# Kernel optimization log

Hardware: AMD Instinct MI355X
Metric: run time of the kernel (lower is better)

Reference implementation:

```python
import jax, jax.numpy as jnp
import numpy as np

# dims
B, S, LC, K, CE, L, WE, H = 64, 512, 16, 3, 10, 32, 200, 200
V, A, T = 50000, 128, 64
LP = LC + K - 1  # padded word length (pad_word adds (K-1)/2 on each side)
D_IN = WE + L    # LSTM input dim = 232


def setup_inputs() -> dict:
    key = jax.random.key(0)
    ks = jax.random.split(key, 16)
    f = lambda k, shp: jax.random.normal(k, shp, dtype=jnp.float32) * 0.05
    return {
        "char_ids": jax.random.randint(ks[0], (B, S, LP), 0, A),
        "word_ids": jax.random.randint(ks[1], (B, S), 0, V),
        "word_emb": f(ks[2], (V, WE)),
        "char_emb": f(ks[3], (A, CE)),
        "conv_w": f(ks[4], (L, K * CE)),   # Conv1d(1, l, K*CE) == linear 30->32
        "conv_b": f(ks[5], (L,)),
        "w_ih_f": f(ks[6], (4 * H, D_IN)),
        "w_hh_f": f(ks[7], (4 * H, H)),
        "b_ih_f": f(ks[8], (4 * H,)),
        "b_hh_f": f(ks[9], (4 * H,)),
        "w_ih_b": f(ks[10], (4 * H, D_IN)),
        "w_hh_b": f(ks[11], (4 * H, H)),
        "b_ih_b": f(ks[12], (4 * H,)),
        "b_hh_b": f(ks[13], (4 * H,)),
        "out_w": f(ks[14], (T, 2 * H)),
        "out_b": f(ks[15], (T,)),
    }


def _lstm(x, w_ih, w_hh, b_ih, b_hh, reverse):
    # x: [S, B, D]; PyTorch gate order i, f, g, o
    def step(carry, x_t):
        h, c = carry
        g = x_t @ w_ih.T + b_ih + h @ w_hh.T + b_hh
        i, f, gg, o = jnp.split(g, 4, axis=-1)
        c = jax.nn.sigmoid(f) * c + jax.nn.sigmoid(i) * jnp.tanh(gg)
        h = jax.nn.sigmoid(o) * jnp.tanh(c)
        return (h, c), h

    b = x.shape[1]
    init = (jnp.zeros((b, H), x.dtype), jnp.zeros((b, H), x.dtype))
    _, hs = jax.lax.scan(step, init, x, reverse=reverse)
    return hs  # [S, B, H]


def reference(char_ids, word_ids, word_emb, char_emb, conv_w, conv_b,
              w_ih_f, w_hh_f, b_ih_f, b_hh_f,
              w_ih_b, w_hh_b, b_ih_b, b_hh_b,
              out_w, out_b):
    # per-word char CNN + max-pool, fully batched over (B, S, windows)
    ce = char_emb[char_ids]                                    # [B,S,LP,CE]
    # sliding K-char windows, flattened to K*CE (== original x_hat construction)
    win = jnp.concatenate([ce[:, :, k:k + LC] for k in range(K)], axis=-1)  # [B,S,LC,K*CE]
    phi = jnp.einsum('bswd,ld->bswl', win, conv_w) + conv_b    # tiny conv == linear
    char_repr = phi.max(axis=2)                                # max-pool over positions -> [B,S,L]

    combined = jnp.concatenate([word_emb[word_ids], char_repr], axis=-1)  # [B,S,232]
    x = combined.reshape(S, B, D_IN)  # faithful to original .view (reshape, not transpose)

    hf = _lstm(x, w_ih_f, w_hh_f, b_ih_f, b_hh_f, reverse=False)
    hb = _lstm(x, w_ih_b, w_hh_b, b_ih_b, b_hh_b, reverse=True)
    lstm_out = jnp.concatenate([hf, hb], axis=-1)              # [S,B,2H]  (dropout: eval mode)

    tag_space = lstm_out.reshape(B, S, 2 * H) @ out_w.T + out_b  # faithful .view back
    return jax.nn.log_softmax(tag_space, axis=1)  # original normalizes over dim=1 (seq axis)
```

## Files before the change

kernel.cpp:

```cpp
#include <hip/hip_runtime.h>
#include <hip/hip_bf16.h>
#include <math.h>

constexpr int B_ = 64, S_ = 512, LP_ = 18, CE_ = 10, LF_ = 32;
constexpr int WE_ = 200, H_ = 200, T_ = 64;
constexpr int N_ = B_ * S_;
constexpr int KP_ = 256;
constexpr int G4_ = 800;
constexpr int NG_ = 1600;
constexpr int NGP_ = 1664;
constexpr float L2E_ = 1.4426950408889634f;

typedef short short8 __attribute__((ext_vector_type(8)));
typedef float f32x4 __attribute__((ext_vector_type(4)));

__device__ __forceinline__ ushort bf16bits(float v) {
  return __bfloat16_as_ushort(__float2bfloat16(v));
}
__device__ __forceinline__ float bf2f(ushort u) {
  return __uint_as_float(((uint)u) << 16);
}
__device__ __forceinline__ float exp2fast(float x) {
  float r; asm("v_exp_f32 %0, %1" : "=v"(r) : "v"(x)); return r;
}
__device__ __forceinline__ float sig2(float y) {
  return __builtin_amdgcn_rcpf(1.f + exp2fast(-y));
}

__global__ __launch_bounds__(256) void k_build_x(
    const int* __restrict__ char_ids, const int* __restrict__ word_ids,
    const float* __restrict__ word_emb, const float* __restrict__ char_emb,
    const float* __restrict__ conv_w, const float* __restrict__ conv_b,
    ushort* __restrict__ Xb)
{
  __shared__ float ce[4][LP_ * CE_];
  const int wave = threadIdx.x >> 6, lane = threadIdx.x & 63;
  const int n = blockIdx.x * 4 + wave;

  for (int i = lane; i < LP_ * CE_; i += 64) {
    int c = char_ids[n * LP_ + i / CE_];
    ce[wave][i] = char_emb[c * CE_ + (i % CE_)];
  }
  const float* we = word_emb + (size_t)word_ids[n] * WE_;
  ushort* xr = Xb + (size_t)n * KP_;
  if (lane < 50) {
    float4 p = *(const float4*)(we + lane * 4);
    ushort4 o;
    o.x = bf16bits(p.x); o.y = bf16bits(p.y); o.z = bf16bits(p.z); o.w = bf16bits(p.w);
    *(ushort4*)(xr + lane * 4) = o;
  }
  if (lane < KP_ - WE_ - LF_) xr[WE_ + LF_ + lane] = 0;
  __syncthreads();

  const int f = lane & 31, half = lane >> 5;
  float cw[30];
  #pragma unroll
  for (int i = 0; i < 30; ++i) cw[i] = conv_w[f * 30 + i];
  float m = -1e30f;
  for (int w = half * 8; w < half * 8 + 8; ++w) {
    float acc = 0.f;
    #pragma unroll
    for (int i = 0; i < 30; ++i) acc += ce[wave][w * CE_ + i] * cw[i];
    m = fmaxf(m, acc);
  }
  m = fmaxf(m, __shfl_xor(m, 32));
  if (half == 0) xr[WE_ + f] = bf16bits(m + conv_b[f]);
}

__global__ __launch_bounds__(64) void k_pack_w(
    const float* __restrict__ w_ih_f, const float* __restrict__ w_ih_b,
    const float* __restrict__ b_ih_f, const float* __restrict__ b_hh_f,
    const float* __restrict__ b_ih_b, const float* __restrict__ b_hh_b,
    ushort* __restrict__ Wb, float* __restrict__ biasc)
{
  const int r = blockIdx.x;
  if (r >= NG_) {
    for (int c = threadIdx.x; c < KP_; c += 64) Wb[(size_t)r * KP_ + c] = 0;
    if (threadIdx.x == 0) biasc[r] = 0.f;
    return;
  }
  const int rl = r < G4_ ? r : r - G4_;
  const int gate = rl / 200;
  const float sc = (gate == 2) ? 2.f * L2E_ : L2E_;
  const float* src = r < G4_ ? w_ih_f + (size_t)rl * 232 : w_ih_b + (size_t)rl * 232;
  for (int c = threadIdx.x; c < KP_; c += 64)
    Wb[(size_t)r * KP_ + c] = (c < 232) ? bf16bits(src[c] * sc) : (ushort)0;
  if (threadIdx.x == 0)
    biasc[r] = sc * (r < G4_ ? (b_ih_f[rl] + b_hh_f[rl]) : (b_ih_b[rl] + b_hh_b[rl]));
}

__global__ __launch_bounds__(64) void k_pack_wo(
    const float* __restrict__ out_w, ushort* __restrict__ Wo)
{
  const int r = blockIdx.x;
  for (int k = threadIdx.x; k < 416; k += 64)
    Wo[(size_t)r * 416 + k] = (k < 400) ? bf16bits(out_w[(size_t)r * 400 + k]) : (ushort)0;
}

__global__ __launch_bounds__(512) void k_gemm_proj(
    const ushort* __restrict__ Xb, const ushort* __restrict__ Wb,
    const float* __restrict__ biasc, ushort* __restrict__ Gc)
{
  __shared__ __align__(16) char smem[131072];
  const int tid = threadIdx.x;
  const int lane = tid & 63, w = tid >> 6;
  const int wr = w >> 2, wc = w & 3;
  const int colbase = blockIdx.x * 128;
  const int rowbase = blockIdx.y * 128;

  const char* Ag = (const char*)(Xb + (size_t)rowbase * KP_);
  const char* Bg = (const char*)(Wb + (size_t)colbase * KP_);
  #pragma unroll
  for (int it = 0; it < 8; ++it) {
    int slot = it * 512 + tid;
    int row = slot >> 5, c16 = slot & 31;
    int src = row * 512 + c16 * 16;
    int dst = row * 512 + ((c16 * 16) ^ ((row & 7) << 4));
    *(short8*)(smem + dst) = *(const short8*)(Ag + src);
    *(short8*)(smem + 65536 + dst) = *(const short8*)(Bg + src);
  }
  __syncthreads();

  f32x4 acc[4][2] = {};
  #pragma unroll
  for (int kk = 0; kk < 8; ++kk) {
    const int kb = kk * 64 + (lane >> 4) * 16;
    short8 a[4], b[2];
    #pragma unroll
    for (int m = 0; m < 4; ++m) {
      int ar = wr * 64 + m * 16 + (lane & 15);
      a[m] = *(const short8*)(smem + ar * 512 + (kb ^ ((ar & 7) << 4)));
    }
    #pragma unroll
    for (int n = 0; n < 2; ++n) {
      int bc = wc * 32 + n * 16 + (lane & 15);
      b[n] = *(const short8*)(smem + 65536 + bc * 512 + (kb ^ ((bc & 7) << 4)));
    }
    #pragma unroll
    for (int m = 0; m < 4; ++m)
      #pragma unroll
      for (int n = 0; n < 2; ++n)
        acc[m][n] = __builtin_amdgcn_mfma_f32_16x16x32_bf16(a[m], b[n], acc[m][n], 0, 0, 0);
  }
  __syncthreads();

  float* Cs = (float*)smem;
  #pragma unroll
  for (int m = 0; m < 4; ++m)
    #pragma unroll
    for (int n = 0; n < 2; ++n)
      #pragma unroll
      for (int i = 0; i < 4; ++i) {
        int r = wr * 64 + m * 16 + (lane >> 4) * 4 + i;
        int c = wc * 32 + n * 16 + (lane & 15);
        Cs[r * 132 + c] = acc[m][n][i];
      }
  __syncthreads();

  const int r = tid >> 2, cg = (tid & 3) * 32;
  ushort ob[32];
  #pragma unroll
  for (int j = 0; j < 32; ++j)
    ob[j] = bf16bits(Cs[r * 132 + cg + j] + biasc[colbase + cg + j]);
  const int colg = colbase + cg;
  ushort* dst = Gc + (size_t)(rowbase + r) * NG_ + colg;
  #pragma unroll
  for (int v = 0; v < 4; ++v)
    if (colg + v * 8 < NG_)
      *(short8*)(dst + v * 8) = *(short8*)(ob + v * 8);
}

__global__ __launch_bounds__(1024) void k_lstm(
    const ushort* __restrict__ Gc,
    const float* __restrict__ w_hh_f, const float* __restrict__ w_hh_b,
    ushort* __restrict__ hf, ushort* __restrict__ hb)
{
  __shared__ ushort h_lds[2][16][232];
  __shared__ __align__(16) char wlds45[2][65536];
  __shared__ __align__(16) char wlds6[17408];

  const int tid = threadIdx.x;
  const int lane = tid & 63, w = tid >> 6;
  const int lo = lane & 15, hi = lane >> 4;
  const bool hiHalf = lo >= 8;
  const int dir = blockIdx.x >> 3, grp = blockIdx.x & 7;
  const float* Whh = dir ? w_hh_b : w_hh_f;
  ushort* hout = dir ? hb : hf;

  for (int i = tid; i < 2 * 16 * 232; i += 1024) ((ushort*)h_lds)[i] = 0;
  if (tid < 256) ((uint*)(wlds6 + 16384))[tid] = 0;

  const int s = w;
  const int off = s < 12 ? 12 * s : 144 + 16 * (s - 12);
  const int cnt = s < 12 ? 12 : 16;
  const int rl  = min(cnt, 200 - off);

  short8 wreg[4][4];
  #pragma unroll
  for (int g = 0; g < 4; ++g) {
    const float sc = (g == 2) ? 2.f * L2E_ : L2E_;
    const float* wr = Whh + (size_t)(g * 200 + off + lo) * 200;
    const bool rowok = lo < rl;
    const int gid = s * 4 + g;
    #pragma unroll
    for (int kt = 0; kt < 7; ++kt) {
      const int k0 = kt * 32 + hi * 8;
      float v[8];
      if (rowok && k0 < 200) {
        float4 p0 = *(const float4*)(wr + k0);
        float4 p1 = *(const float4*)(wr + k0 + 4);
        v[0] = p0.x; v[1] = p0.y; v[2] = p0.z; v[3] = p0.w;
        v[4] = p1.x; v[5] = p1.y; v[6] = p1.z; v[7] = p1.w;
      } else {
        #pragma unroll
        for (int j = 0; j < 8; ++j) v[j] = 0.f;
      }
      short8 fr;
      #pragma unroll
      for (int j = 0; j < 8; ++j) fr[j] = (short)bf16bits(v[j] * sc);
      if (kt < 4) wreg[g][kt] = fr;
      else if (kt < 6) *(short8*)(wlds45[kt - 4] + gid * 1024 + lane * 16) = fr;
      else if (hi == 0) *(short8*)(wlds6 + gid * 256 + lo * 16) = fr;
    }
  }

  float c2_[2] = {0.f, 0.f};

  const int rowsel = lo & 7;
  const int step0 = dir ? (S_ - 1) : 0;
  const ushort* gpp = Gc + (size_t)(step0 * 64 + grp * 8 + rowsel) * NG_ + dir * G4_ + off + hi * 4;
  ushort* sp = hout + (size_t)(step0 * 64 + grp * 8 + rowsel) * H_ + off + hi * 4 + (hiHalf ? 2 : 0);
  const ptrdiff_t gstep = (dir ? -64 : 64) * (ptrdiff_t)NG_;
  const ptrdiff_t hstep = (dir ? -64 : 64) * (ptrdiff_t)H_;
  const bool cellok = (hi * 4 < rl);
  const int hwoff = rowsel * 464 + off * 2 + hi * 8 + (hiHalf ? 4 : 0);

  const char* base45a = wlds45[0] + s * 4096 + lane * 16;
  const char* base45b = wlds45[1] + s * 4096 + lane * 16;
  const char* base6   = wlds6 + ((hi == 0) ? (s * 1024 + lo * 16) : (16384 + lo * 16));

  __syncthreads();

  #pragma unroll 2
  for (int t = 0; t < S_; ++t) {
    const ushort (*HR)[232] = h_lds[t & 1];
    ushort (*HW)[232] = h_lds[(t & 1) ^ 1];

    uint2 pre[4];
    #pragma unroll
    for (int g = 0; g < 4; ++g)
      pre[g] = *(const uint2*)(gpp + g * 200);

    __builtin_amdgcn_s_setprio(1);
    f32x4 acc[4] = {};
    const char* hrow = (const char*)HR + lo * 464 + hi * 16;
    #pragma unroll
    for (int kt = 0; kt < 7; ++kt) {
      short8 hfr = *(const short8*)(hrow + kt * 64);
      if (kt < 4) {
        #pragma unroll
        for (int g = 0; g < 4; ++g)
          acc[g] = __builtin_amdgcn_mfma_f32_16x16x32_bf16(wreg[g][kt], hfr, acc[g], 0, 0, 0);
      } else if (kt == 4) {
        #pragma unroll
        for (int g = 0; g < 4; ++g) {
          short8 wk = *(const short8*)(base45a + g * 1024);
          acc[g] = __builtin_amdgcn_mfma_f32_16x16x32_bf16(wk, hfr, acc[g], 0, 0, 0);
        }
      } else if (kt == 5) {
        #pragma unroll
        for (int g = 0; g < 4; ++g) {
          short8 wk = *(const short8*)(base45b + g * 1024);
          acc[g] = __builtin_amdgcn_mfma_f32_16x16x32_bf16(wk, hfr, acc[g], 0, 0, 0);
        }
      } else {
        #pragma unroll
        for (int g = 0; g < 4; ++g) {
          short8 wk = *(const short8*)(base6 + g * 256);
          acc[g] = __builtin_amdgcn_mfma_f32_16x16x32_bf16(wk, hfr, acc[g], 0, 0, 0);
        }
      }
    }
    __builtin_amdgcn_s_setprio(0);

    const uint ui = hiHalf ? pre[0].y : pre[0].x;
    const uint uf = hiHalf ? pre[1].y : pre[1].x;
    const uint ug = hiHalf ? pre[2].y : pre[2].x;
    const uint uo = hiHalf ? pre[3].y : pre[3].x;
    const float aI0 = hiHalf ? acc[0][2] : acc[0][0];
    const float aI1 = hiHalf ? acc[0][3] : acc[0][1];
    const float aF0 = hiHalf ? acc[1][2] : acc[1][0];
    const float aF1 = hiHalf ? acc[1][3] : acc[1][1];
    const float aG0 = hiHalf ? acc[2][2] : acc[2][0];
    const float aG1 = hiHalf ? acc[2][3] : acc[2][1];
    const float aO0 = hiHalf ? acc[3][2] : acc[3][0];
    const float aO1 = hiHalf ? acc[3][3] : acc[3][1];

    float hv0, hv1;
    {
      float gi = aI0 + bf2f((ushort)ui);
      float gf = aF0 + bf2f((ushort)uf);
      float gg = aG0 + bf2f((ushort)ug);
      float go = aO0 + bf2f((ushort)uo);
      float cn = sig2(gf) * c2_[0] + sig2(gi) * (2.f * sig2(gg) - 1.f);
      c2_[0] = cn;
      hv0 = sig2(go) * (2.f * sig2(cn * (2.f * L2E_)) - 1.f);
    }
    {
      float gi = aI1 + bf2f((ushort)(ui >> 16));
      float gf = aF1 + bf2f((ushort)(uf >> 16));
      float gg = aG1 + bf2f((ushort)(ug >> 16));
      float go = aO1 + bf2f((ushort)(uo >> 16));
      float cn = sig2(gf) * c2_[1] + sig2(gi) * (2.f * sig2(gg) - 1.f);
      c2_[1] = cn;
      hv1 = sig2(go) * (2.f * sig2(cn * (2.f * L2E_)) - 1.f);
    }
    const uint pkw = (uint)bf16bits(hv0) | ((uint)bf16bits(hv1) << 16);
    if (cellok) {
      *(uint*)((char*)HW + hwoff) = pkw;
    }

    __syncthreads();

    if (cellok) *(uint*)sp = pkw;
    sp += hstep;
    gpp += gstep;
  }
}

__global__ __launch_bounds__(256) void k_out(
    const ushort* __restrict__ hf, const ushort* __restrict__ hb,
    const ushort* __restrict__ Wo, const float* __restrict__ out_b,
    float* __restrict__ tag)
{
  __shared__ __align__(16) char smem[131072];
  const int tid = threadIdx.x;
  const int lane = tid & 63, w = tid >> 6;
  const int n0 = blockIdx.x * 64;

  for (int s2 = tid; s2 < 64 * 52; s2 += 256) {
    int row = s2 / 52, c = s2 % 52;
    short8 v = {};
    if (c < 25)      v = *(const short8*)(hf + (size_t)(n0 + row) * H_ + c * 8);
    else if (c < 50) v = *(const short8*)(hb + (size_t)(n0 + row) * H_ + (c - 25) * 8);
    *(short8*)(smem + row * 1024 + ((c ^ (row & 7)) << 4)) = v;
  }
  for (int s2 = tid; s2 < 64 * 52; s2 += 256) {
    int row = s2 / 52, c = s2 % 52;
    short8 v = *(const short8*)(Wo + (size_t)row * 416 + c * 8);
    *(short8*)(smem + 65536 + row * 1024 + ((c ^ (row & 7)) << 4)) = v;
  }
  __syncthreads();

  const int lo4 = lane & 15, hi4 = lane >> 4;
  f32x4 acc[4] = {};
  #pragma unroll
  for (int kt = 0; kt < 13; ++kt) {
    const int ck = kt * 4 + hi4;
    const int ar = w * 16 + lo4;
    short8 a = *(const short8*)(smem + ar * 1024 + ((ck ^ (ar & 7)) << 4));
    #pragma unroll
    for (int n = 0; n < 4; ++n) {
      const int br = n * 16 + lo4;
      short8 b = *(const short8*)(smem + 65536 + br * 1024 + ((ck ^ (br & 7)) << 4));
      acc[n] = __builtin_amdgcn_mfma_f32_16x16x32_bf16(a, b, acc[n], 0, 0, 0);
    }
  }
  #pragma unroll
  for (int n = 0; n < 4; ++n) {
    const int col = n * 16 + lo4;
    const float bb = out_b[col];
    #pragma unroll
    for (int i = 0; i < 4; ++i) {
      const int row = hi4 * 4 + i;
      tag[(size_t)(n0 + w * 16 + row) * T_ + col] = acc[n][i] + bb;
    }
  }
}

__global__ __launch_bounds__(256) void k_lsm(
    const float* __restrict__ tag, float* __restrict__ out)
{
  __shared__ float red[4][T_];
  __shared__ float lse[T_];
  const int b = blockIdx.x;
  const int tt = threadIdx.x & 63, ch = threadIdx.x >> 6;
  const float* tb = tag + (size_t)b * S_ * T_;

  float m = -1e30f;
  for (int s = ch * 128; s < ch * 128 + 128; ++s) m = fmaxf(m, tb[s * T_ + tt]);
  red[ch][tt] = m;
  __syncthreads();
  if (ch == 0)
    lse[tt] = fmaxf(fmaxf(red[0][tt], red[1][tt]), fmaxf(red[2][tt], red[3][tt]));
  __syncthreads();
  m = lse[tt];
  float sum = 0.f;
  for (int s = ch * 128; s < ch * 128 + 128; ++s) sum += __expf(tb[s * T_ + tt] - m);
  __syncthreads();
  red[ch][tt] = sum;
  __syncthreads();
  if (ch == 0)
    lse[tt] = m + logf(red[0][tt] + red[1][tt] + red[2][tt] + red[3][tt]);
  __syncthreads();
  const float l = lse[tt];
  float* ob = out + (size_t)b * S_ * T_;
  for (int s = ch * 128; s < ch * 128 + 128; ++s) ob[s * T_ + tt] = tb[s * T_ + tt] - l;
}

extern "C" void kernel_launch(void* const* d_in, const int* in_sizes, int n_in,
                              void* d_out, int out_size, void* d_ws, size_t ws_size,
                              hipStream_t stream) {
  const int*   char_ids = (const int*)d_in[0];
  const int*   word_ids = (const int*)d_in[1];
  const float* word_emb = (const float*)d_in[2];
  const float* char_emb = (const float*)d_in[3];
  const float* conv_w   = (const float*)d_in[4];
  const float* conv_b   = (const float*)d_in[5];
  const float* w_ih_f   = (const float*)d_in[6];
  const float* w_hh_f   = (const float*)d_in[7];
  const float* b_ih_f   = (const float*)d_in[8];
  const float* b_hh_f   = (const float*)d_in[9];
  const float* w_ih_b   = (const float*)d_in[10];
  const float* w_hh_b   = (const float*)d_in[11];
  const float* b_ih_b   = (const float*)d_in[12];
  const float* b_hh_b   = (const float*)d_in[13];
  const float* out_w    = (const float*)d_in[14];
  const float* out_b    = (const float*)d_in[15];

  char* ws = (char*)d_ws;
  ushort* Xb    = (ushort*)(ws);
  ushort* Wb    = (ushort*)(ws + 16777216);
  float*  biasc = (float*) (ws + 17629184);
  ushort* Wo    = (ushort*)(ws + 17635840);
  ushort* Gc    = (ushort*)(ws + 18422016);
  ushort* hf    = (ushort*)(ws + 123279616);
  ushort* hb    = (ushort*)(ws + 136386816);
  float*  tag   = (float*) (ws + 149494016);

  hipLaunchKernelGGL(k_build_x, dim3(N_ / 4), dim3(256), 0, stream,
                     char_ids, word_ids, word_emb, char_emb, conv_w, conv_b, Xb);
  hipLaunchKernelGGL(k_pack_w, dim3(NGP_), dim3(64), 0, stream,
                     w_ih_f, w_ih_b, b_ih_f, b_hh_f, b_ih_b, b_hh_b, Wb, biasc);
  hipLaunchKernelGGL(k_pack_wo, dim3(T_), dim3(64), 0, stream, out_w, Wo);
  hipLaunchKernelGGL(k_gemm_proj, dim3(NGP_ / 128, N_ / 128), dim3(512), 0, stream,
                     Xb, Wb, biasc, Gc);
  hipLaunchKernelGGL(k_lstm, dim3(16), dim3(1024), 0, stream, Gc, w_hh_f, w_hh_b, hf, hb);
  hipLaunchKernelGGL(k_out, dim3(N_ / 64), dim3(256), 0, stream, hf, hb, Wo, out_b, tag);
  hipLaunchKernelGGL(k_lsm, dim3(B_), dim3(256), 0, stream, tag, (float*)d_out);
}
```

Baseline: 1.418 ms.

## Fuse output projection with seq-axis log-softmax and merge weight packing kernels

The output GEMM and the log-softmax over the sequence axis now run in one kernel, one block per batch element. Each block keeps all 512x64 logits in registers and does the max and sum reductions through shared memory, so the fp32 tag buffer is never written to or read back from global memory. Packing of the output weights also moves into the input-weight packing kernel, which removes one launch. In exchange the fused kernel runs only 64 blocks with heavy register use, which lowers parallelism for the GEMM part.

```diff
diff --git a/kernel.cpp b/kernel.cpp
--- a/kernel.cpp
+++ b/kernel.cpp
@@ -71,9 +71,16 @@
     const float* __restrict__ w_ih_f, const float* __restrict__ w_ih_b,
     const float* __restrict__ b_ih_f, const float* __restrict__ b_hh_f,
     const float* __restrict__ b_ih_b, const float* __restrict__ b_hh_b,
-    ushort* __restrict__ Wb, float* __restrict__ biasc)
+    const float* __restrict__ out_w,
+    ushort* __restrict__ Wb, float* __restrict__ biasc, ushort* __restrict__ Wo)
 {
   const int r = blockIdx.x;
+  if (r >= NGP_) {
+    const int r2 = r - NGP_;
+    for (int k = threadIdx.x; k < 416; k += 64)
+      Wo[(size_t)r2 * 416 + k] = (k < 400) ? bf16bits(out_w[(size_t)r2 * 400 + k]) : (ushort)0;
+    return;
+  }
   if (r >= NG_) {
     for (int c = threadIdx.x; c < KP_; c += 64) Wb[(size_t)r * KP_ + c] = 0;
     if (threadIdx.x == 0) biasc[r] = 0.f;
@@ -87,14 +94,6 @@
     Wb[(size_t)r * KP_ + c] = (c < 232) ? bf16bits(src[c] * sc) : (ushort)0;
   if (threadIdx.x == 0)
     biasc[r] = sc * (r < G4_ ? (b_ih_f[rl] + b_hh_f[rl]) : (b_ih_b[rl] + b_hh_b[rl]));
-}
-
-__global__ __launch_bounds__(64) void k_pack_wo(
-    const float* __restrict__ out_w, ushort* __restrict__ Wo)
-{
-  const int r = blockIdx.x;
-  for (int k = threadIdx.x; k < 416; k += 64)
-    Wo[(size_t)r * 416 + k] = (k < 400) ? bf16bits(out_w[(size_t)r * 400 + k]) : (ushort)0;
 }
 
 __global__ __launch_bounds__(512) void k_gemm_proj(
@@ -328,84 +327,115 @@
   }
 }
 
-__global__ __launch_bounds__(256) void k_out(
+__global__ __launch_bounds__(512) void k_out_lsm(
     const ushort* __restrict__ hf, const ushort* __restrict__ hb,
     const ushort* __restrict__ Wo, const float* __restrict__ out_b,
-    float* __restrict__ tag)
+    float* __restrict__ out)
 {
-  __shared__ __align__(16) char smem[131072];
+  __shared__ __align__(16) char Bs[65536];
+  __shared__ __align__(16) char As[65536];
+  __shared__ float red[64][17];
+  __shared__ float mf[64], lsef[64];
+
   const int tid = threadIdx.x;
   const int lane = tid & 63, w = tid >> 6;
-  const int n0 = blockIdx.x * 64;
-
-  for (int s2 = tid; s2 < 64 * 52; s2 += 256) {
+  const int lo4 = lane & 15, hi4 = lane >> 4;
+  const int rfrag = w & 3;
+  const int cpair = (w >> 2) * 2;
+  const int b = blockIdx.x;
+  const size_t n0 = (size_t)b * S_;
+
+  for (int s2 = tid; s2 < 64 * 52; s2 += 512) {
     int row = s2 / 52, c = s2 % 52;
-    short8 v = {};
-    if (c < 25)      v = *(const short8*)(hf + (size_t)(n0 + row) * H_ + c * 8);
-    else if (c < 50) v = *(const short8*)(hb + (size_t)(n0 + row) * H_ + (c - 25) * 8);
-    *(short8*)(smem + row * 1024 + ((c ^ (row & 7)) << 4)) = v;
-  }
-  for (int s2 = tid; s2 < 64 * 52; s2 += 256) {
-    int row = s2 / 52, c = s2 % 52;
-    short8 v = *(const short8*)(Wo + (size_t)row * 416 + c * 8);
-    *(short8*)(smem + 65536 + row * 1024 + ((c ^ (row & 7)) << 4)) = v;
-  }
-  __syncthreads();
-
-  const int lo4 = lane & 15, hi4 = lane >> 4;
-  f32x4 acc[4] = {};
-  #pragma unroll
-  for (int kt = 0; kt < 13; ++kt) {
-    const int ck = kt * 4 + hi4;
-    const int ar = w * 16 + lo4;
-    short8 a = *(const short8*)(smem + ar * 1024 + ((ck ^ (ar & 7)) << 4));
-    #pragma unroll
-    for (int n = 0; n < 4; ++n) {
-      const int br = n * 16 + lo4;
-      short8 b = *(const short8*)(smem + 65536 + br * 1024 + ((ck ^ (br & 7)) << 4));
-      acc[n] = __builtin_amdgcn_mfma_f32_16x16x32_bf16(a, b, acc[n], 0, 0, 0);
-    }
-  }
-  #pragma unroll
-  for (int n = 0; n < 4; ++n) {
-    const int col = n * 16 + lo4;
-    const float bb = out_b[col];
-    #pragma unroll
-    for (int i = 0; i < 4; ++i) {
-      const int row = hi4 * 4 + i;
-      tag[(size_t)(n0 + w * 16 + row) * T_ + col] = acc[n][i] + bb;
-    }
-  }
-}
-
-__global__ __launch_bounds__(256) void k_lsm(
-    const float* __restrict__ tag, float* __restrict__ out)
-{
-  __shared__ float red[4][T_];
-  __shared__ float lse[T_];
-  const int b = blockIdx.x;
-  const int tt = threadIdx.x & 63, ch = threadIdx.x >> 6;
-  const float* tb = tag + (size_t)b * S_ * T_;
-
-  float m = -1e30f;
-  for (int s = ch * 128; s < ch * 128 + 128; ++s) m = fmaxf(m, tb[s * T_ + tt]);
-  red[ch][tt] = m;
-  __syncthreads();
-  if (ch == 0)
-    lse[tt] = fmaxf(fmaxf(red[0][tt], red[1][tt]), fmaxf(red[2][tt], red[3][tt]));
-  __syncthreads();
-  m = lse[tt];
-  float sum = 0.f;
-  for (int s = ch * 128; s < ch * 128 + 128; ++s) sum += __expf(tb[s * T_ + tt] - m);
-  __syncthreads();
-  red[ch][tt] = sum;
-  __syncthreads();
-  if (ch == 0)
-    lse[tt] = m + logf(red[0][tt] + red[1][tt] + red[2][tt] + red[3][tt]);
-  __syncthreads();
-  const float l = lse[tt];
-  float* ob = out + (size_t)b * S_ * T_;
-  for (int s = ch * 128; s < ch * 128 + 128; ++s) ob[s * T_ + tt] = tb[s * T_ + tt] - l;
+    *(short8*)(Bs + row * 1024 + ((c ^ (row & 7)) << 4)) =
+        *(const short8*)(Wo + (size_t)row * 416 + c * 8);
+  }
+
+  f32x4 acc[8][2] = {};
+  #pragma unroll
+  for (int it = 0; it < 8; ++it) {
+    __syncthreads();
+    for (int s2 = tid; s2 < 64 * 52; s2 += 512) {
+      int row = s2 / 52, c = s2 % 52;
+      short8 v = {};
+      const size_t n = n0 + it * 64 + row;
+      if (c < 25)      v = *(const short8*)(hf + n * H_ + c * 8);
+      else if (c < 50) v = *(const short8*)(hb + n * H_ + (c - 25) * 8);
+      *(short8*)(As + row * 1024 + ((c ^ (row & 7)) << 4)) = v;
+    }
+    __syncthreads();
+    #pragma unroll
+    for (int kt = 0; kt < 13; ++kt) {
+      const int ck = kt * 4 + hi4;
+      const int ar = rfrag * 16 + lo4;
+      short8 a = *(const short8*)(As + ar * 1024 + ((ck ^ (ar & 7)) << 4));
+      #pragma unroll
+      for (int cc = 0; cc < 2; ++cc) {
+        const int br = (cpair + cc) * 16 + lo4;
+        short8 bv = *(const short8*)(Bs + br * 1024 + ((ck ^ (br & 7)) << 4));
+        acc[it][cc] = __builtin_amdgcn_mfma_f32_16x16x32_bf16(a, bv, acc[it][cc], 0, 0, 0);
+      }
+    }
+  }
+
+  #pragma unroll
+  for (int cc = 0; cc < 2; ++cc) {
+    const float bb = out_b[(cpair + cc) * 16 + lo4];
+    #pragma unroll
+    for (int it = 0; it < 8; ++it)
+      #pragma unroll
+      for (int i = 0; i < 4; ++i) acc[it][cc][i] += bb;
+  }
+
+  #pragma unroll
+  for (int cc = 0; cc < 2; ++cc) {
+    float pm = -1e30f;
+    #pragma unroll
+    for (int it = 0; it < 8; ++it)
+      #pragma unroll
+      for (int i = 0; i < 4; ++i) pm = fmaxf(pm, acc[it][cc][i]);
+    red[(cpair + cc) * 16 + lo4][rfrag * 4 + hi4] = pm;
+  }
+  __syncthreads();
+  if (tid < 64) {
+    float m = red[tid][0];
+    #pragma unroll
+    for (int k = 1; k < 16; ++k) m = fmaxf(m, red[tid][k]);
+    mf[tid] = m;
+  }
+  __syncthreads();
+
+  #pragma unroll
+  for (int cc = 0; cc < 2; ++cc) {
+    const float m = mf[(cpair + cc) * 16 + lo4];
+    float ps = 0.f;
+    #pragma unroll
+    for (int it = 0; it < 8; ++it)
+      #pragma unroll
+      for (int i = 0; i < 4; ++i) ps += exp2fast((acc[it][cc][i] - m) * L2E_);
+    red[(cpair + cc) * 16 + lo4][rfrag * 4 + hi4] = ps;
+  }
+  __syncthreads();
+  if (tid < 64) {
+    float ssum = 0.f;
+    #pragma unroll
+    for (int k = 0; k < 16; ++k) ssum += red[tid][k];
+    lsef[tid] = mf[tid] + logf(ssum);
+  }
+  __syncthreads();
+
+  #pragma unroll
+  for (int cc = 0; cc < 2; ++cc) {
+    const int t = (cpair + cc) * 16 + lo4;
+    const float l = lsef[t];
+    #pragma unroll
+    for (int it = 0; it < 8; ++it)
+      #pragma unroll
+      for (int i = 0; i < 4; ++i) {
+        const int sidx = it * 64 + rfrag * 16 + hi4 * 4 + i;
+        out[(n0 + sidx) * T_ + t] = acc[it][cc][i] - l;
+      }
+  }
 }
 
 extern "C" void kernel_launch(void* const* d_in, const int* in_sizes, int n_in,
@@ -436,16 +466,13 @@
   ushort* Gc    = (ushort*)(ws + 18422016);
   ushort* hf    = (ushort*)(ws + 123279616);
   ushort* hb    = (ushort*)(ws + 136386816);
-  float*  tag   = (float*) (ws + 149494016);
 
   hipLaunchKernelGGL(k_build_x, dim3(N_ / 4), dim3(256), 0, stream,
                      char_ids, word_ids, word_emb, char_emb, conv_w, conv_b, Xb);
-  hipLaunchKernelGGL(k_pack_w, dim3(NGP_), dim3(64), 0, stream,
-                     w_ih_f, w_ih_b, b_ih_f, b_hh_f, b_ih_b, b_hh_b, Wb, biasc);
-  hipLaunchKernelGGL(k_pack_wo, dim3(T_), dim3(64), 0, stream, out_w, Wo);
+  hipLaunchKernelGGL(k_pack_w, dim3(NGP_ + T_), dim3(64), 0, stream,
+                     w_ih_f, w_ih_b, b_ih_f, b_hh_f, b_ih_b, b_hh_b, out_w, Wb, biasc, Wo);
   hipLaunchKernelGGL(k_gemm_proj, dim3(NGP_ / 128, N_ / 128), dim3(512), 0, stream,
                      Xb, Wb, biasc, Gc);
   hipLaunchKernelGGL(k_lstm, dim3(16), dim3(1024), 0, stream, Gc, w_hh_f, w_hh_b, hf, hb);
-  hipLaunchKernelGGL(k_out, dim3(N_ / 64), dim3(256), 0, stream, hf, hb, Wo, out_b, tag);
-  hipLaunchKernelGGL(k_lsm, dim3(B_), dim3(256), 0, stream, tag, (float*)d_out);
-}
+  hipLaunchKernelGGL(k_out_lsm, dim3(B_), dim3(512), 0, stream, hf, hb, Wo, out_b, (float*)d_out);
+}
```

Measured after the change: 1.411 ms. Within noise of the previous version (-0.5%).
